# Performance work log

Hardware: AMD Instinct MI355X
Metric: run time of the kernel (lower is better)

Reference implementation:

```python
import jax, jax.numpy as jnp
import numpy as np
import math

D_MODEL = 512
NHEAD = 8
NUM_LAYERS = 3
FF_HIDDEN = 512
B, LQ, LK = 4, 1024, 2048
LN_EPS = 1e-5


def _mha(q_in, k_in, v_in, Wq, Wk, Wv, Wo, nhead, mask):
    # Weights stored [d_in, d_out]; torch Linear(bias=False) is x @ W.T, we fold the
    # transpose into storage so math is identical.
    Bq, Lq, d = q_in.shape
    dh = d // nhead
    # NOTE: original uses .view(B, nhead, -1, dh) on contiguous [B, L, d] — a plain
    # row-major reshape, NOT the usual transpose head split. Replicate exactly.
    q = (q_in @ Wq).reshape(Bq, nhead, -1, dh)
    k = (k_in @ Wk).reshape(Bq, nhead, -1, dh)
    v = (v_in @ Wv).reshape(Bq, nhead, -1, dh)
    u = jnp.einsum('bhqd,bhkd->bhqk', q, k) / math.sqrt(dh)
    if mask is not None:
        m = mask[:, None]  # broadcast over heads
        u = jnp.where(m, -jnp.inf, u)
    attn = jax.nn.softmax(u, axis=-1)
    if mask is not None:
        attn = jnp.where(m, 0.0, attn)
    out = jnp.einsum('bhqk,bhkd->bhqd', attn, v).reshape(Bq, Lq, d)
    return out @ Wo


def _layernorm(x, g, b):
    mu = jnp.mean(x, axis=-1, keepdims=True)
    var = jnp.mean((x - mu) ** 2, axis=-1, keepdims=True)
    return (x - mu) * jax.lax.rsqrt(var + LN_EPS) * g + b


def setup_inputs() -> dict:
    key = jax.random.key(0)
    ks = jax.random.split(key, 16)
    d, L, f = D_MODEL, NUM_LAYERS, FF_HIDDEN
    s = 0.02
    inp = {
        'x': jax.random.normal(ks[0], (B, LK, d), jnp.float32),
        'h': jax.random.normal(ks[1], (B, LQ, d), jnp.float32),
        'mask': jax.random.randint(ks[2], (B, LQ, LK), 0, 10) == 0,
        'wq': jax.random.normal(ks[3], (L, d, d), jnp.float32) * s,
        'wk': jax.random.normal(ks[4], (L, d, d), jnp.float32) * s,
        'wv': jax.random.normal(ks[5], (L, d, d), jnp.float32) * s,
        'wo': jax.random.normal(ks[6], (L, d, d), jnp.float32) * s,
        'ffw1': jax.random.normal(ks[7], (L, d, f), jnp.float32) * s,
        'ffb1': jnp.zeros((L, f), jnp.float32),
        'ffw2': jax.random.normal(ks[8], (L, f, d), jnp.float32) * s,
        'ffb2': jnp.zeros((L, d), jnp.float32),
        'g1': jnp.ones((L, d), jnp.float32),
        'be1': jnp.zeros((L, d), jnp.float32),
        'g2': jnp.ones((L, d), jnp.float32),
        'be2': jnp.zeros((L, d), jnp.float32),
        'out_wq': jax.random.normal(ks[9], (d, d), jnp.float32) * s,
        'out_wk': jax.random.normal(ks[10], (d, d), jnp.float32) * s,
    }
    return inp


def reference(x, h, mask, wq, wk, wv, wo, ffw1, ffb1, ffw2, ffb2, g1, be1, g2, be2, out_wq, out_wk):
    L = wq.shape[0]
    for i in range(L):
        a = _mha(h, x, x, wq[i], wk[i], wv[i], wo[i], NHEAD, mask)
        h = _layernorm(h + a, g1[i], be1[i])
        ff = jax.nn.relu(h @ ffw1[i] + ffb1[i]) @ ffw2[i] + ffb2[i]
        h = _layernorm(h + ff, g2[i], be2[i])
    # output MHA with nhead=1, output_attention=True: returns u.mean(dim=1)
    d = h.shape[-1]
    q = (h @ out_wq)[:, None]  # [B,1,Lq,d]
    k = (x @ out_wk)[:, None]  # [B,1,Lk,d]
    u = jnp.einsum('bhqd,bhkd->bhqk', q, k) / math.sqrt(d)
    # mean over head dim of size 1; torch .squeeze(1) is a no-op since Lq > 1
    return u.mean(axis=1)  # [B, Lq, Lk]
```

## Files before the change

kernel.cpp:

```cpp
#include <hip/hip_runtime.h>
#include <math.h>


#define D_MODEL 512
#define LQ 1024
#define LKK 2048
#define BB 4
#define NL 3
#define KSPLIT 2
#define NROWS 32768

typedef __bf16 bf16;
typedef __bf16 bf16x8 __attribute__((ext_vector_type(8)));
typedef __bf16 bf16x4 __attribute__((ext_vector_type(4)));
typedef float f32x4 __attribute__((ext_vector_type(4)));

__device__ inline f32x4 mfma16(bf16x8 a, bf16x8 b, f32x4 c) {
    return __builtin_amdgcn_mfma_f32_16x16x32_bf16(a, b, c, 0, 0, 0);
}

__device__ inline void gload16(const void* g, void* l) {
    __builtin_amdgcn_global_load_lds(
        (const __attribute__((address_space(1))) void*)g,
        (__attribute__((address_space(3))) void*)l, 16, 0, 0);
}

__global__ __launch_bounds__(256) void cast_kernel(
    const float* __restrict__ in, bf16* __restrict__ out, long n)
{
    long i4 = ((long)blockIdx.x * 256 + threadIdx.x) * 4;
    if (i4 >= n) return;
    float4 v = *(const float4*)(in + i4);
    bf16x4 o;
    o[0] = (bf16)v.x; o[1] = (bf16)v.y; o[2] = (bf16)v.z; o[3] = (bf16)v.w;
    *(bf16x4*)(out + i4) = o;
}

__global__ __launch_bounds__(256) void tcast_kernel(
    const float* __restrict__ in, bf16* __restrict__ out, long dstride)
{
    __shared__ float t[32][33];
    const float* ip = in + (long)blockIdx.z * 262144;
    bf16* op = out + (long)blockIdx.z * dstride;
    int tx = threadIdx.x & 31, ty = threadIdx.x >> 5;
    int x0 = blockIdx.x * 32, y0 = blockIdx.y * 32;
#pragma unroll
    for (int i = 0; i < 4; i++)
        t[ty + 8 * i][tx] = ip[(long)(y0 + ty + 8 * i) * 512 + x0 + tx];
    __syncthreads();
#pragma unroll
    for (int i = 0; i < 4; i++)
        op[(long)(x0 + ty + 8 * i) * 512 + y0 + tx] = (bf16)t[tx][ty + 8 * i];
}

__global__ __launch_bounds__(256) void maskbits_kernel(
    const int* __restrict__ m, unsigned* __restrict__ bits)
{
    long i = (long)blockIdx.x * 256 + threadIdx.x;
    int v = m[i] != 0;
    unsigned long long bal = __ballot(v);
    int lane = threadIdx.x & 63;
    if (lane == 0) bits[i >> 5] = (unsigned)bal;
    else if (lane == 32) bits[i >> 5] = (unsigned)(bal >> 32);
}

__global__ __launch_bounds__(256) void vtrans_kernel(
    const bf16* __restrict__ v, bf16* __restrict__ vt)
{
    __shared__ bf16 t[64][72];
    int bh = blockIdx.y;
    int p0 = blockIdx.x * 64;
    const bf16* vb = v + ((long)bh * 2048 + p0) * 64;
    bf16* vtb = vt + (long)bh * 64 * 2048;
    int tid = threadIdx.x;
#pragma unroll
    for (int it = 0; it < 2; it++) {
        int r = it * 32 + (tid >> 3);
        int c8 = (tid & 7) * 8;
        bf16x8 vv = *(const bf16x8*)(vb + (long)r * 64 + c8);
        *(bf16x8*)&t[r][c8] = vv;
    }
    __syncthreads();
#pragma unroll
    for (int it = 0; it < 2; it++) {
        int d = it * 32 + (tid >> 3);
        int p8 = (tid & 7) * 8;
        bf16x8 ov;
#pragma unroll
        for (int j = 0; j < 8; j++) ov[j] = t[p8 + j][d];
        *(bf16x8*)(vtb + (long)d * 2048 + p0 + p8) = ov;
    }
}

template<int BIAS, int RELU, int OUT_BF16>
__global__ __launch_bounds__(256) void mfma_gemm(
    const bf16* __restrict__ A, const bf16* __restrict__ Bt,
    const float* __restrict__ bias, void* __restrict__ Cv,
    int N, int K, float scale, long sA, long sB, long sC)
{
    __shared__ bf16 As[128][32];
    __shared__ bf16 Bs[64][32];
    int tid = threadIdx.x;
    int lane = tid & 63, w = tid >> 6;
    int wr = w >> 1, wc = w & 1;
    int g = lane >> 4, c = lane & 15;
    long z = blockIdx.z;
    const bf16* Ab = A + z * sA;
    const bf16* Bb = Bt + z * sB;
    long row0 = (long)blockIdx.y * 128;
    int n0 = blockIdx.x * 64;

    f32x4 acc[4][2];
#pragma unroll
    for (int m = 0; m < 4; m++)
#pragma unroll
        for (int n = 0; n < 2; n++) acc[m][n] = (f32x4){0.f, 0.f, 0.f, 0.f};

    for (int k0 = 0; k0 < K; k0 += 32) {
        __syncthreads();
        const bf16* ga = Ab + (row0 + w * 32 + (lane >> 2)) * K + k0 + (lane & 3) * 8;
        gload16(ga, &As[w * 32][0]);
        gload16(ga + (long)16 * K, &As[w * 32 + 16][0]);
        const bf16* gb = Bb + (long)(n0 + w * 16 + (lane >> 2)) * K + k0 + (lane & 3) * 8;
        gload16(gb, &Bs[w * 16][0]);
        __syncthreads();
        bf16x8 af[4], bfr[2];
#pragma unroll
        for (int m = 0; m < 4; m++)
            af[m] = *(const bf16x8*)&As[wr * 64 + m * 16 + c][g * 8];
#pragma unroll
        for (int n = 0; n < 2; n++)
            bfr[n] = *(const bf16x8*)&Bs[wc * 32 + n * 16 + c][g * 8];
#pragma unroll
        for (int m = 0; m < 4; m++)
#pragma unroll
            for (int n = 0; n < 2; n++)
                acc[m][n] = mfma16(af[m], bfr[n], acc[m][n]);
    }

    float bv[2] = {0.f, 0.f};
    if (BIAS) {
#pragma unroll
        for (int n = 0; n < 2; n++) bv[n] = bias[n0 + wc * 32 + n * 16 + c];
    }
    float* Cf = (float*)Cv + z * sC;
    bf16* Cb = (bf16*)Cv + z * sC;
#pragma unroll
    for (int m = 0; m < 4; m++)
#pragma unroll
        for (int n = 0; n < 2; n++)
#pragma unroll
            for (int j = 0; j < 4; j++) {
                long row = row0 + wr * 64 + m * 16 + g * 4 + j;
                int col = n0 + wc * 32 + n * 16 + c;
                float v = acc[m][n][j] * scale;
                if (BIAS) v += bv[n];
                if (RELU) v = fmaxf(v, 0.f);
                if (OUT_BF16) Cb[row * N + col] = (bf16)v;
                else Cf[row * N + col] = v;
            }
}

template<int OUT_BF16>
__global__ __launch_bounds__(256) void mfma_gemm128(
    const bf16* __restrict__ A, const bf16* __restrict__ Bt,
    void* __restrict__ Cv, int N, int K, float scale,
    long sA, long sB, long sC)
{
    __shared__ bf16 As[128][32];
    __shared__ bf16 Bs[128][32];
    int tid = threadIdx.x;
    int lane = tid & 63, w = tid >> 6;
    int wr = w >> 1, wc = w & 1;
    int g = lane >> 4, c = lane & 15;
    long z = blockIdx.z;
    const bf16* Ab = A + z * sA;
    const bf16* Bb = Bt + z * sB;
    long row0 = (long)blockIdx.y * 128;
    int n0 = blockIdx.x * 128;

    f32x4 acc[4][4];
#pragma unroll
    for (int m = 0; m < 4; m++)
#pragma unroll
        for (int n = 0; n < 4; n++) acc[m][n] = (f32x4){0.f, 0.f, 0.f, 0.f};

    for (int k0 = 0; k0 < K; k0 += 32) {
        __syncthreads();
        const bf16* ga = Ab + (row0 + w * 16 + (lane >> 2)) * K + k0 + (lane & 3) * 8;
        gload16(ga, &As[w * 16][0]);
        gload16(ga + (long)64 * K, &As[w * 16 + 64][0]);
        const bf16* gb = Bb + (long)(n0 + w * 16 + (lane >> 2)) * K + k0 + (lane & 3) * 8;
        gload16(gb, &Bs[w * 16][0]);
        gload16(gb + (long)64 * K, &Bs[w * 16 + 64][0]);
        __syncthreads();
        bf16x8 af[4], bfr[4];
#pragma unroll
        for (int m = 0; m < 4; m++)
            af[m] = *(const bf16x8*)&As[wr * 64 + m * 16 + c][g * 8];
#pragma unroll
        for (int n = 0; n < 4; n++)
            bfr[n] = *(const bf16x8*)&Bs[wc * 64 + n * 16 + c][g * 8];
#pragma unroll
        for (int m = 0; m < 4; m++)
#pragma unroll
            for (int n = 0; n < 4; n++)
                acc[m][n] = mfma16(af[m], bfr[n], acc[m][n]);
    }

    float* Cf = (float*)Cv + z * sC;
    bf16* Cb = (bf16*)Cv + z * sC;
#pragma unroll
    for (int m = 0; m < 4; m++)
#pragma unroll
        for (int n = 0; n < 4; n++)
#pragma unroll
            for (int j = 0; j < 4; j++) {
                long row = row0 + wr * 64 + m * 16 + g * 4 + j;
                int col = n0 + wc * 64 + n * 16 + c;
                float v = acc[m][n][j] * scale;
                if (OUT_BF16) Cb[row * N + col] = (bf16)v;
                else Cf[row * N + col] = v;
            }
}

__global__ __launch_bounds__(256, 4) void attn_mfma(
    const bf16* __restrict__ QP, const bf16* __restrict__ KP,
    const bf16* __restrict__ Vt, const unsigned* __restrict__ bits,
    bf16* __restrict__ Opart, float* __restrict__ Mpart,
    float* __restrict__ Lpart)
{
    __shared__ bf16 Kls[2][4096];
    __shared__ bf16 Vls[2][4096];
    __shared__ bf16 Pl[4][1024];

    int tid = threadIdx.x;
    int lane = tid & 63, wv = tid >> 6;
    int g = lane >> 4, c = lane & 15;

    int flat = blockIdx.x;
    int logical = (flat & 7) * 128 + (flat >> 3);
    int bh = logical >> 5;
    int rr = logical & 31;
    int sp = rr >> 4;
    int q0 = (rr & 15) * 64 + wv * 16;
    int b = bh >> 3;

    long qrow0 = (long)bh * 1024 + q0;
    long krow0 = (long)bh * 2048 + (long)sp * 1024;
    const bf16* vtb = Vt + (long)bh * 131072 + (long)sp * 1024;
    const unsigned* bitrow = bits + ((long)b * 1024 + q0 + c) * 64 + sp * 32;

    int lr = lane >> 3, lc = lane & 7;
    int scol = (lc ^ lr) * 8;
    int cs = c & 7;

    bf16x8 qa[2];
#pragma unroll
    for (int hh = 0; hh < 2; hh++)
        qa[hh] = *(const bf16x8*)(QP + (qrow0 + c) * 64 + hh * 32 + g * 8);

    f32x4 o_acc[4];
#pragma unroll
    for (int ot = 0; ot < 4; ot++) o_acc[ot] = (f32x4){0.f, 0.f, 0.f, 0.f};
    float m_r = -1e30f, l_r = 0.f;

    {
        const bf16* sk = KP + (krow0 + wv * 16 + lr) * 64 + scol;
        gload16(sk, &Kls[0][(wv * 16) * 64]);
        gload16(sk + 8 * 64, &Kls[0][(wv * 16 + 8) * 64]);
        const bf16* sv = vtb + (long)(wv * 16 + lr) * 2048 + scol;
        gload16(sv, &Vls[0][(wv * 16) * 64]);
        gload16(sv + 8 * 2048, &Vls[0][(wv * 16 + 8) * 64]);
    }
    uint2 wp_nxt = *(const uint2*)(bitrow);
    __syncthreads();

    const int NT = LKK / KSPLIT / 64;
    for (int kt = 0; kt < NT; kt++) {
        int cur = kt & 1;
        if (kt + 1 < NT) {
            int kn = (kt + 1) * 64;
            const bf16* sk = KP + (krow0 + kn + wv * 16 + lr) * 64 + scol;
            gload16(sk, &Kls[cur ^ 1][(wv * 16) * 64]);
            gload16(sk + 8 * 64, &Kls[cur ^ 1][(wv * 16 + 8) * 64]);
            const bf16* sv = vtb + (long)(wv * 16 + lr) * 2048 + kn + scol;
            gload16(sv, &Vls[cur ^ 1][(wv * 16) * 64]);
            gload16(sv + 8 * 2048, &Vls[cur ^ 1][(wv * 16 + 8) * 64]);
        }
        uint2 wp = wp_nxt;
        if (kt + 1 < NT) wp_nxt = *(const uint2*)(bitrow + (kt + 1) * 2);

        const char* kls = (const char*)&Kls[cur][0];
        f32x4 s[4];
#pragma unroll
        for (int mt = 0; mt < 4; mt++) {
            bf16x8 ka0 = *(const bf16x8*)(kls + (mt * 16 + c) * 128 + ((g ^ cs) << 4));
            bf16x8 ka1 = *(const bf16x8*)(kls + (mt * 16 + c) * 128 + (((4 + g) ^ cs) << 4));
            s[mt] = mfma16(ka0, qa[0], (f32x4){0.f, 0.f, 0.f, 0.f});
            s[mt] = mfma16(ka1, qa[1], s[mt]);
        }

#pragma unroll
        for (int mt = 0; mt < 4; mt++)
#pragma unroll
            for (int j = 0; j < 4; j++) {
                int kl = mt * 16 + 4 * g + j;
                unsigned wsel = (kl < 32) ? wp.x : wp.y;
                s[mt][j] = ((wsel >> (kl & 31)) & 1) ? -1e30f : s[mt][j] * 0.125f;
            }

        float mx = -1e30f;
#pragma unroll
        for (int mt = 0; mt < 4; mt++)
            mx = fmaxf(mx, fmaxf(fmaxf(s[mt][0], s[mt][1]),
                                 fmaxf(s[mt][2], s[mt][3])));
        mx = fmaxf(mx, __shfl_xor(mx, 16, 64));
        mx = fmaxf(mx, __shfl_xor(mx, 32, 64));

        float fct = 1.f;
        if (__any(mx > m_r + 8.f)) {
            float mnew = fmaxf(m_r, mx);
            fct = __expf(m_r - mnew);
            m_r = mnew;
            float fq[4];
#pragma unroll
            for (int j = 0; j < 4; j++)
                fq[j] = __shfl(fct, (lane & 48) | (4 * g + j), 64);
#pragma unroll
            for (int ot = 0; ot < 4; ot++)
#pragma unroll
                for (int j = 0; j < 4; j++) o_acc[ot][j] *= fq[j];
        }

        float sum = 0.f;
#pragma unroll
        for (int mt = 0; mt < 4; mt++)
#pragma unroll
            for (int j = 0; j < 4; j++) {
                float p = __expf(s[mt][j] - m_r);
                s[mt][j] = p;
                sum += p;
            }
        sum += __shfl_xor(sum, 16, 64);
        sum += __shfl_xor(sum, 32, 64);
        l_r = l_r * fct + sum;

        char* plb = (char*)&Pl[wv][0];
#pragma unroll
        for (int mt = 0; mt < 4; mt++) {
            bf16x4 pk;
#pragma unroll
            for (int j = 0; j < 4; j++) pk[j] = (bf16)s[mt][j];
            int wch = (mt * 2 + (g >> 1)) ^ cs;
            *(bf16x4*)(plb + c * 128 + (wch << 4) + (g & 1) * 8) = pk;
        }

        const char* vls = (const char*)&Vls[cur][0];
#pragma unroll
        for (int kh = 0; kh < 2; kh++) {
            bf16x8 pa = *(const bf16x8*)(plb + c * 128 + ((((kh << 2) + g) ^ cs) << 4));
#pragma unroll
            for (int ot = 0; ot < 4; ot++) {
                bf16x8 vbf = *(const bf16x8*)
                    (vls + (ot * 16 + c) * 128 + ((((kh << 2) + g) ^ cs) << 4));
                o_acc[ot] = mfma16(pa, vbf, o_acc[ot]);
            }
        }
        __syncthreads();
    }

    long ob = ((long)sp * NROWS + qrow0) * 64;
#pragma unroll
    for (int ot = 0; ot < 4; ot++)
#pragma unroll
        for (int j = 0; j < 4; j++)
            Opart[ob + (long)(4 * g + j) * 64 + ot * 16 + c] = (bf16)o_acc[ot][j];
    if (g == 0) {
        Mpart[(long)sp * NROWS + qrow0 + c] = m_r;
        Lpart[(long)sp * NROWS + qrow0 + c] = l_r;
    }
}

__global__ __launch_bounds__(256) void attn_combine(
    const bf16* __restrict__ Op, const float* __restrict__ Mp,
    const float* __restrict__ Lp, bf16* __restrict__ O)
{
    long idx = (long)blockIdx.x * 256 + threadIdx.x;
    long row = idx >> 6;
    float m0 = Mp[row], m1 = Mp[NROWS + row];
    float l0 = Lp[row], l1 = Lp[NROWS + row];
    float mm = fmaxf(m0, m1);
    float e0 = __expf(m0 - mm), e1 = __expf(m1 - mm);
    float inv = 1.f / (l0 * e0 + l1 * e1);
    float o = ((float)Op[idx] * e0 + (float)Op[(long)NROWS * 64 + idx] * e1) * inv;
    O[idx] = (bf16)o;
}

__global__ __launch_bounds__(256) void ln_kernel(
    const float* __restrict__ res, const float* __restrict__ y,
    const float* __restrict__ g, const float* __restrict__ bb,
    float* __restrict__ outf, bf16* __restrict__ outb)
{
    int wave = threadIdx.x >> 6, lane = threadIdx.x & 63;
    long row = (long)blockIdx.x * 4 + wave;
    const float* rp = res + row * D_MODEL;
    const float* yp = y + row * D_MODEL;
    float v[8];
    float s = 0.f, sq = 0.f;
#pragma unroll
    for (int j = 0; j < 8; j++) {
        int col = lane + 64 * j;
        v[j] = rp[col] + yp[col];
        s += v[j]; sq += v[j] * v[j];
    }
#pragma unroll
    for (int o = 32; o > 0; o >>= 1) {
        s += __shfl_down(s, o, 64);
        sq += __shfl_down(sq, o, 64);
    }
    s = __shfl(s, 0, 64);
    sq = __shfl(sq, 0, 64);
    float mean = s * (1.f / 512.f);
    float var = sq * (1.f / 512.f) - mean * mean;
    float rstd = rsqrtf(fmaxf(var, 0.f) + 1e-5f);
    float* opf = outf + row * D_MODEL;
    bf16* opb = outb + row * D_MODEL;
#pragma unroll
    for (int j = 0; j < 8; j++) {
        int col = lane + 64 * j;
        float o = (v[j] - mean) * rstd * g[col] + bb[col];
        opf[col] = o;
        opb[col] = (bf16)o;
    }
}

extern "C" void kernel_launch(void* const* d_in, const int* in_sizes, int n_in,
                              void* d_out, int out_size, void* d_ws, size_t ws_size,
                              hipStream_t stream)
{
    const float* x    = (const float*)d_in[0];
    const float* hin  = (const float*)d_in[1];
    const int*   mask = (const int*)d_in[2];
    const float* wq   = (const float*)d_in[3];
    const float* wk   = (const float*)d_in[4];
    const float* wv   = (const float*)d_in[5];
    const float* wo   = (const float*)d_in[6];
    const float* ffw1 = (const float*)d_in[7];
    const float* ffb1 = (const float*)d_in[8];
    const float* ffw2 = (const float*)d_in[9];
    const float* ffb2 = (const float*)d_in[10];
    const float* g1   = (const float*)d_in[11];
    const float* be1  = (const float*)d_in[12];
    const float* g2   = (const float*)d_in[13];
    const float* be2  = (const float*)d_in[14];
    const float* out_wq = (const float*)d_in[15];
    const float* out_wk = (const float*)d_in[16];
    float* out = (float*)d_out;

    const long NQ = (long)BB * LQ;
    const long NK = (long)BB * LKK;
    const long WSZ = 512L * 512;

    char* W = (char*)d_ws;
    float* h_f  = (float*)(W);
    char*  SH   = W + 8388608;
    float* y_f  = (float*)SH;
    bf16*  v_pl = (bf16*)SH;
    bf16*  opart= (bf16*)SH;
    bf16*  h_b  = (bf16*)(W + 16777216);
    bf16*  x_b  = (bf16*)(W + 20971520);
    bf16*  q_b  = (bf16*)(W + 29360128);
    bf16*  a_b  = (bf16*)(W + 33554432);
    bf16*  k_pl = (bf16*)(W + 37748736);
    bf16*  vt   = (bf16*)(W + 46137344);
    bf16*  wts  = (bf16*)(W + 54525952);
    bf16*  wtQ  = wts;
    bf16*  wtO  = wts + 3 * WSZ;
    bf16*  wtF1 = wts + 6 * WSZ;
    bf16*  wtF2 = wts + 9 * WSZ;
    bf16*  wtKV = wts + 12 * WSZ;
    bf16*  wtOQ = wts + 19 * WSZ;
    unsigned* mb = (unsigned*)(W + 65011712);
    float* Mpart = (float*)(W + 66060288);
    float* Lpart = (float*)(W + 66322432);

    const long sKV = ((bf16*)SH) - k_pl;

    dim3 blk(256);

    hipMemcpyAsync(h_f, hin, NQ * D_MODEL * sizeof(float),
                   hipMemcpyDeviceToDevice, stream);
    cast_kernel<<<dim3((NK * D_MODEL / 4 + 255) / 256), blk, 0, stream>>>(x, x_b, NK * D_MODEL);
    cast_kernel<<<dim3((NQ * D_MODEL / 4 + 255) / 256), blk, 0, stream>>>(hin, h_b, NQ * D_MODEL);
    dim3 gt(16, 16, 3);
    tcast_kernel<<<gt, blk, 0, stream>>>(wq, wtQ, WSZ);
    tcast_kernel<<<gt, blk, 0, stream>>>(wo, wtO, WSZ);
    tcast_kernel<<<gt, blk, 0, stream>>>(ffw1, wtF1, WSZ);
    tcast_kernel<<<gt, blk, 0, stream>>>(ffw2, wtF2, WSZ);
    tcast_kernel<<<gt, blk, 0, stream>>>(wk, wtKV, 2 * WSZ);
    tcast_kernel<<<gt, blk, 0, stream>>>(wv, wtKV + WSZ, 2 * WSZ);
    dim3 gt1(16, 16, 1);
    tcast_kernel<<<gt1, blk, 0, stream>>>(out_wk, wtKV + 6 * WSZ, 0);
    tcast_kernel<<<gt1, blk, 0, stream>>>(out_wq, wtOQ, 0);
    maskbits_kernel<<<dim3(32768), blk, 0, stream>>>(mask, mb);

    dim3 gq(8, 32, 1);
    dim3 gkv(4, 64, 2);
    dim3 gvt(32, 32);
    dim3 ga(1024);
    dim3 gc(NROWS * 64 / 256);

    for (int i = 0; i < NL; i++) {
        mfma_gemm<0,0,1><<<gq, blk, 0, stream>>>(h_b, wtQ + i * WSZ, nullptr, q_b,
            512, 512, 1.f, 0, 0, 0);
        mfma_gemm128<1><<<gkv, blk, 0, stream>>>(x_b, wtKV + 2 * i * WSZ, k_pl,
            512, 512, 1.f, 0, WSZ, sKV);
        vtrans_kernel<<<gvt, blk, 0, stream>>>(v_pl, vt);

        attn_mfma<<<ga, blk, 0, stream>>>(q_b, k_pl, vt, mb, opart, Mpart, Lpart);
        attn_combine<<<gc, blk, 0, stream>>>(opart, Mpart, Lpart, a_b);

        mfma_gemm<0,0,0><<<gq, blk, 0, stream>>>(a_b, wtO + i * WSZ, nullptr, y_f,
            512, 512, 1.f, 0, 0, 0);
        ln_kernel<<<dim3(NQ / 4), blk, 0, stream>>>(h_f, y_f,
            g1 + i * D_MODEL, be1 + i * D_MODEL, h_f, h_b);

        mfma_gemm<1,1,1><<<gq, blk, 0, stream>>>(h_b, wtF1 + i * WSZ,
            ffb1 + i * D_MODEL, q_b, 512, 512, 1.f, 0, 0, 0);
        mfma_gemm<1,0,0><<<gq, blk, 0, stream>>>(q_b, wtF2 + i * WSZ,
            ffb2 + i * D_MODEL, y_f, 512, 512, 1.f, 0, 0, 0);
        ln_kernel<<<dim3(NQ / 4), blk, 0, stream>>>(h_f, y_f,
            g2 + i * D_MODEL, be2 + i * D_MODEL, h_f, h_b);
    }

    mfma_gemm<0,0,1><<<gq, blk, 0, stream>>>(h_b, wtOQ, nullptr, q_b,
        512, 512, 1.f, 0, 0, 0);
    dim3 gkf(4, 64, 1);
    mfma_gemm128<1><<<gkf, blk, 0, stream>>>(x_b, wtKV + 6 * WSZ, k_pl,
        512, 512, 1.f, 0, 0, 0);
    dim3 gf(LKK / 128, LQ / 128, BB);
    mfma_gemm128<0><<<gf, blk, 0, stream>>>(q_b, k_pl, out,
        LKK, 512, 0.04419417382415922f,
        (long)LQ * 512, (long)LKK * 512, (long)LQ * LKK);
}
```

Before: 475.3 us.

## Double-buffer GEMM LDS tiles, fuse QKV projections, merge weight casts, use exp2

Both GEMM kernels now double-buffer their LDS tiles, so the next K-slice is prefetched while MFMAs run on the current one, leaving one barrier per iteration. The Q, K and V projections per layer, and the final Q/K projections, go through a single fused 128-tile kernel launch instead of separate launches. The eight weight transpose-cast launches become one kernel, and attention softmax switches to exp2 with the log2e factor folded into the scale and rescale threshold. The costs are twice the LDS per block, which may lower occupancy, and branchy per-z dispatch inside the fused kernels.

```diff
diff --git a/kernel.cpp b/kernel.cpp
--- a/kernel.cpp
+++ b/kernel.cpp
@@ -9,6 +9,7 @@
 #define NL 3
 #define KSPLIT 2
 #define NROWS 32768
+#define WSZC 262144L
 
 typedef __bf16 bf16;
 typedef __bf16 bf16x8 __attribute__((ext_vector_type(8)));
@@ -36,21 +37,34 @@
     *(bf16x4*)(out + i4) = o;
 }
 
-__global__ __launch_bounds__(256) void tcast_kernel(
-    const float* __restrict__ in, bf16* __restrict__ out, long dstride)
+__global__ __launch_bounds__(256) void tcast_all(
+    const float* __restrict__ wq, const float* __restrict__ wo,
+    const float* __restrict__ f1, const float* __restrict__ f2,
+    const float* __restrict__ wk, const float* __restrict__ wv,
+    const float* __restrict__ owq, const float* __restrict__ owk,
+    bf16* __restrict__ wts, bf16* __restrict__ wtOQ)
 {
     __shared__ float t[32][33];
-    const float* ip = in + (long)blockIdx.z * 262144;
-    bf16* op = out + (long)blockIdx.z * dstride;
+    int z = blockIdx.z;
+    const float* src; bf16* dst;
+    if (z < 3)       { src = wq  + z * WSZC;        dst = wts + (long)z * WSZC; }
+    else if (z < 6)  { src = wo  + (z - 3) * WSZC;  dst = wts + (long)z * WSZC; }
+    else if (z < 9)  { src = f1  + (z - 6) * WSZC;  dst = wts + (long)z * WSZC; }
+    else if (z < 12) { src = f2  + (z - 9) * WSZC;  dst = wts + (long)z * WSZC; }
+    else if (z < 15) { src = wk  + (z - 12) * WSZC; dst = wts + (12 + 2 * (z - 12)) * WSZC; }
+    else if (z < 18) { src = wv  + (z - 15) * WSZC; dst = wts + (13 + 2 * (z - 15)) * WSZC; }
+    else if (z == 18){ src = owq;                   dst = wtOQ; }
+    else             { src = owk;                   dst = wts + 18 * WSZC; }
+
     int tx = threadIdx.x & 31, ty = threadIdx.x >> 5;
     int x0 = blockIdx.x * 32, y0 = blockIdx.y * 32;
 #pragma unroll
     for (int i = 0; i < 4; i++)
-        t[ty + 8 * i][tx] = ip[(long)(y0 + ty + 8 * i) * 512 + x0 + tx];
+        t[ty + 8 * i][tx] = src[(long)(y0 + ty + 8 * i) * 512 + x0 + tx];
     __syncthreads();
 #pragma unroll
     for (int i = 0; i < 4; i++)
-        op[(long)(x0 + ty + 8 * i) * 512 + y0 + tx] = (bf16)t[tx][ty + 8 * i];
+        dst[(long)(x0 + ty + 8 * i) * 512 + y0 + tx] = (bf16)t[tx][ty + 8 * i];
 }
 
 __global__ __launch_bounds__(256) void maskbits_kernel(
@@ -96,17 +110,14 @@
 __global__ __launch_bounds__(256) void mfma_gemm(
     const bf16* __restrict__ A, const bf16* __restrict__ Bt,
     const float* __restrict__ bias, void* __restrict__ Cv,
-    int N, int K, float scale, long sA, long sB, long sC)
-{
-    __shared__ bf16 As[128][32];
-    __shared__ bf16 Bs[64][32];
+    int N, int K)
+{
+    __shared__ bf16 As[2][4096];
+    __shared__ bf16 Bs[2][2048];
     int tid = threadIdx.x;
     int lane = tid & 63, w = tid >> 6;
     int wr = w >> 1, wc = w & 1;
     int g = lane >> 4, c = lane & 15;
-    long z = blockIdx.z;
-    const bf16* Ab = A + z * sA;
-    const bf16* Bb = Bt + z * sB;
     long row0 = (long)blockIdx.y * 128;
     int n0 = blockIdx.x * 64;
 
@@ -116,26 +127,34 @@
 #pragma unroll
         for (int n = 0; n < 2; n++) acc[m][n] = (f32x4){0.f, 0.f, 0.f, 0.f};
 
-    for (int k0 = 0; k0 < K; k0 += 32) {
-        __syncthreads();
-        const bf16* ga = Ab + (row0 + w * 32 + (lane >> 2)) * K + k0 + (lane & 3) * 8;
-        gload16(ga, &As[w * 32][0]);
-        gload16(ga + (long)16 * K, &As[w * 32 + 16][0]);
-        const bf16* gb = Bb + (long)(n0 + w * 16 + (lane >> 2)) * K + k0 + (lane & 3) * 8;
-        gload16(gb, &Bs[w * 16][0]);
-        __syncthreads();
+    int lr4 = lane >> 2, lc8 = (lane & 3) * 8;
+    auto STAGE = [&](int buf, int k0) {
+        const bf16* ga = A + (row0 + w * 32 + lr4) * (long)K + k0 + lc8;
+        gload16(ga, &As[buf][(w * 32) * 32]);
+        gload16(ga + (long)16 * K, &As[buf][(w * 32 + 16) * 32]);
+        const bf16* gb = Bt + (long)(n0 + w * 16 + lr4) * K + k0 + lc8;
+        gload16(gb, &Bs[buf][(w * 16) * 32]);
+    };
+
+    STAGE(0, 0);
+    __syncthreads();
+    int nk = K >> 5;
+    for (int it = 0; it < nk; ++it) {
+        int cur = it & 1;
+        if (it + 1 < nk) STAGE(cur ^ 1, (it + 1) << 5);
         bf16x8 af[4], bfr[2];
 #pragma unroll
         for (int m = 0; m < 4; m++)
-            af[m] = *(const bf16x8*)&As[wr * 64 + m * 16 + c][g * 8];
+            af[m] = *(const bf16x8*)&As[cur][(wr * 64 + m * 16 + c) * 32 + g * 8];
 #pragma unroll
         for (int n = 0; n < 2; n++)
-            bfr[n] = *(const bf16x8*)&Bs[wc * 32 + n * 16 + c][g * 8];
+            bfr[n] = *(const bf16x8*)&Bs[cur][(wc * 32 + n * 16 + c) * 32 + g * 8];
 #pragma unroll
         for (int m = 0; m < 4; m++)
 #pragma unroll
             for (int n = 0; n < 2; n++)
                 acc[m][n] = mfma16(af[m], bfr[n], acc[m][n]);
+        __syncthreads();
     }
 
     float bv[2] = {0.f, 0.f};
@@ -143,8 +162,8 @@
 #pragma unroll
         for (int n = 0; n < 2; n++) bv[n] = bias[n0 + wc * 32 + n * 16 + c];
     }
-    float* Cf = (float*)Cv + z * sC;
-    bf16* Cb = (bf16*)Cv + z * sC;
+    float* Cf = (float*)Cv;
+    bf16* Cb = (bf16*)Cv;
 #pragma unroll
     for (int m = 0; m < 4; m++)
 #pragma unroll
@@ -153,7 +172,7 @@
             for (int j = 0; j < 4; j++) {
                 long row = row0 + wr * 64 + m * 16 + g * 4 + j;
                 int col = n0 + wc * 32 + n * 16 + c;
-                float v = acc[m][n][j] * scale;
+                float v = acc[m][n][j];
                 if (BIAS) v += bv[n];
                 if (RELU) v = fmaxf(v, 0.f);
                 if (OUT_BF16) Cb[row * N + col] = (bf16)v;
@@ -162,22 +181,17 @@
 }
 
 template<int OUT_BF16>
-__global__ __launch_bounds__(256) void mfma_gemm128(
-    const bf16* __restrict__ A, const bf16* __restrict__ Bt,
+__device__ inline void gemm128_body(
+    const bf16* __restrict__ Ab, const bf16* __restrict__ Bb,
     void* __restrict__ Cv, int N, int K, float scale,
-    long sA, long sB, long sC)
-{
-    __shared__ bf16 As[128][32];
-    __shared__ bf16 Bs[128][32];
+    long row0, int n0)
+{
+    __shared__ bf16 As[2][4096];
+    __shared__ bf16 Bs[2][4096];
     int tid = threadIdx.x;
     int lane = tid & 63, w = tid >> 6;
     int wr = w >> 1, wc = w & 1;
     int g = lane >> 4, c = lane & 15;
-    long z = blockIdx.z;
-    const bf16* Ab = A + z * sA;
-    const bf16* Bb = Bt + z * sB;
-    long row0 = (long)blockIdx.y * 128;
-    int n0 = blockIdx.x * 128;
 
     f32x4 acc[4][4];
 #pragma unroll
@@ -185,31 +199,39 @@
 #pragma unroll
         for (int n = 0; n < 4; n++) acc[m][n] = (f32x4){0.f, 0.f, 0.f, 0.f};
 
-    for (int k0 = 0; k0 < K; k0 += 32) {
-        __syncthreads();
-        const bf16* ga = Ab + (row0 + w * 16 + (lane >> 2)) * K + k0 + (lane & 3) * 8;
-        gload16(ga, &As[w * 16][0]);
-        gload16(ga + (long)64 * K, &As[w * 16 + 64][0]);
-        const bf16* gb = Bb + (long)(n0 + w * 16 + (lane >> 2)) * K + k0 + (lane & 3) * 8;
-        gload16(gb, &Bs[w * 16][0]);
-        gload16(gb + (long)64 * K, &Bs[w * 16 + 64][0]);
-        __syncthreads();
+    int lr4 = lane >> 2, lc8 = (lane & 3) * 8;
+    auto STAGE = [&](int buf, int k0) {
+        const bf16* ga = Ab + (row0 + w * 16 + lr4) * (long)K + k0 + lc8;
+        gload16(ga, &As[buf][(w * 16) * 32]);
+        gload16(ga + (long)64 * K, &As[buf][(w * 16 + 64) * 32]);
+        const bf16* gb = Bb + (long)(n0 + w * 16 + lr4) * K + k0 + lc8;
+        gload16(gb, &Bs[buf][(w * 16) * 32]);
+        gload16(gb + (long)64 * K, &Bs[buf][(w * 16 + 64) * 32]);
+    };
+
+    STAGE(0, 0);
+    __syncthreads();
+    int nk = K >> 5;
+    for (int it = 0; it < nk; ++it) {
+        int cur = it & 1;
+        if (it + 1 < nk) STAGE(cur ^ 1, (it + 1) << 5);
         bf16x8 af[4], bfr[4];
 #pragma unroll
         for (int m = 0; m < 4; m++)
-            af[m] = *(const bf16x8*)&As[wr * 64 + m * 16 + c][g * 8];
+            af[m] = *(const bf16x8*)&As[cur][(wr * 64 + m * 16 + c) * 32 + g * 8];
 #pragma unroll
         for (int n = 0; n < 4; n++)
-            bfr[n] = *(const bf16x8*)&Bs[wc * 64 + n * 16 + c][g * 8];
+            bfr[n] = *(const bf16x8*)&Bs[cur][(wc * 64 + n * 16 + c) * 32 + g * 8];
 #pragma unroll
         for (int m = 0; m < 4; m++)
 #pragma unroll
             for (int n = 0; n < 4; n++)
                 acc[m][n] = mfma16(af[m], bfr[n], acc[m][n]);
-    }
-
-    float* Cf = (float*)Cv + z * sC;
-    bf16* Cb = (bf16*)Cv + z * sC;
+        __syncthreads();
+    }
+
+    float* Cf = (float*)Cv;
+    bf16* Cb = (bf16*)Cv;
 #pragma unroll
     for (int m = 0; m < 4; m++)
 #pragma unroll
@@ -224,6 +246,31 @@
             }
 }
 
+__global__ __launch_bounds__(256) void mfma_gemm128(
+    const bf16* __restrict__ A, const bf16* __restrict__ Bt,
+    float* __restrict__ Cv, int N, int K, float scale,
+    long sA, long sB, long sC)
+{
+    long z = blockIdx.z;
+    gemm128_body<0>(A + z * sA, Bt + z * sB, Cv + z * sC, N, K, scale,
+                    (long)blockIdx.y * 128, blockIdx.x * 128);
+}
+
+__global__ __launch_bounds__(256) void qkv_gemm(
+    const bf16* __restrict__ Ah, const bf16* __restrict__ Ax,
+    const bf16* __restrict__ B0, const bf16* __restrict__ B1,
+    const bf16* __restrict__ B2,
+    bf16* __restrict__ C0, bf16* __restrict__ C1, bf16* __restrict__ C2)
+{
+    int z = blockIdx.z;
+    if (z == 0 && blockIdx.y >= 32) return;
+    const bf16* A = z ? Ax : Ah;
+    const bf16* Bt = (z == 0) ? B0 : (z == 1 ? B1 : B2);
+    bf16* C = (z == 0) ? C0 : (z == 1 ? C1 : C2);
+    gemm128_body<1>(A, Bt, C, 512, 512, 1.f,
+                    (long)blockIdx.y * 128, blockIdx.x * 128);
+}
+
 __global__ __launch_bounds__(256, 4) void attn_mfma(
     const bf16* __restrict__ QP, const bf16* __restrict__ KP,
     const bf16* __restrict__ Vt, const unsigned* __restrict__ bits,
@@ -233,6 +280,8 @@
     __shared__ bf16 Kls[2][4096];
     __shared__ bf16 Vls[2][4096];
     __shared__ bf16 Pl[4][1024];
+
+    const float C2 = 0.1803368801111243f;
 
     int tid = threadIdx.x;
     int lane = tid & 63, wv = tid >> 6;
@@ -307,7 +356,7 @@
             for (int j = 0; j < 4; j++) {
                 int kl = mt * 16 + 4 * g + j;
                 unsigned wsel = (kl < 32) ? wp.x : wp.y;
-                s[mt][j] = ((wsel >> (kl & 31)) & 1) ? -1e30f : s[mt][j] * 0.125f;
+                s[mt][j] = ((wsel >> (kl & 31)) & 1) ? -1e30f : s[mt][j] * C2;
             }
 
         float mx = -1e30f;
@@ -319,9 +368,9 @@
         mx = fmaxf(mx, __shfl_xor(mx, 32, 64));
 
         float fct = 1.f;
-        if (__any(mx > m_r + 8.f)) {
+        if (__any(mx > m_r + 11.5415f)) {
             float mnew = fmaxf(m_r, mx);
-            fct = __expf(m_r - mnew);
+            fct = exp2f(m_r - mnew);
             m_r = mnew;
             float fq[4];
 #pragma unroll
@@ -338,7 +387,7 @@
         for (int mt = 0; mt < 4; mt++)
 #pragma unroll
             for (int j = 0; j < 4; j++) {
-                float p = __expf(s[mt][j] - m_r);
+                float p = exp2f(s[mt][j] - m_r);
                 s[mt][j] = p;
                 sum += p;
             }
@@ -391,7 +440,7 @@
     float m0 = Mp[row], m1 = Mp[NROWS + row];
     float l0 = Lp[row], l1 = Lp[NROWS + row];
     float mm = fmaxf(m0, m1);
-    float e0 = __expf(m0 - mm), e1 = __expf(m1 - mm);
+    float e0 = exp2f(m0 - mm), e1 = exp2f(m1 - mm);
     float inv = 1.f / (l0 * e0 + l1 * e1);
     float o = ((float)Op[idx] * e0 + (float)Op[(long)NROWS * 64 + idx] * e1) * inv;
     O[idx] = (bf16)o;
@@ -460,7 +509,6 @@
 
     const long NQ = (long)BB * LQ;
     const long NK = (long)BB * LKK;
-    const long WSZ = 512L * 512;
 
     char* W = (char*)d_ws;
     float* h_f  = (float*)(W);
@@ -475,17 +523,10 @@
     bf16*  k_pl = (bf16*)(W + 37748736);
     bf16*  vt   = (bf16*)(W + 46137344);
     bf16*  wts  = (bf16*)(W + 54525952);
-    bf16*  wtQ  = wts;
-    bf16*  wtO  = wts + 3 * WSZ;
-    bf16*  wtF1 = wts + 6 * WSZ;
-    bf16*  wtF2 = wts + 9 * WSZ;
-    bf16*  wtKV = wts + 12 * WSZ;
-    bf16*  wtOQ = wts + 19 * WSZ;
+    bf16*  wtOQ = wts + 19 * WSZC;
     unsigned* mb = (unsigned*)(W + 65011712);
     float* Mpart = (float*)(W + 66060288);
     float* Lpart = (float*)(W + 66322432);
-
-    const long sKV = ((bf16*)SH) - k_pl;
 
     dim3 blk(256);
 
@@ -493,54 +534,44 @@
                    hipMemcpyDeviceToDevice, stream);
     cast_kernel<<<dim3((NK * D_MODEL / 4 + 255) / 256), blk, 0, stream>>>(x, x_b, NK * D_MODEL);
     cast_kernel<<<dim3((NQ * D_MODEL / 4 + 255) / 256), blk, 0, stream>>>(hin, h_b, NQ * D_MODEL);
-    dim3 gt(16, 16, 3);
-    tcast_kernel<<<gt, blk, 0, stream>>>(wq, wtQ, WSZ);
-    tcast_kernel<<<gt, blk, 0, stream>>>(wo, wtO, WSZ);
-    tcast_kernel<<<gt, blk, 0, stream>>>(ffw1, wtF1, WSZ);
-    tcast_kernel<<<gt, blk, 0, stream>>>(ffw2, wtF2, WSZ);
-    tcast_kernel<<<gt, blk, 0, stream>>>(wk, wtKV, 2 * WSZ);
-    tcast_kernel<<<gt, blk, 0, stream>>>(wv, wtKV + WSZ, 2 * WSZ);
-    dim3 gt1(16, 16, 1);
-    tcast_kernel<<<gt1, blk, 0, stream>>>(out_wk, wtKV + 6 * WSZ, 0);
-    tcast_kernel<<<gt1, blk, 0, stream>>>(out_wq, wtOQ, 0);
+    tcast_all<<<dim3(16, 16, 20), blk, 0, stream>>>(
+        wq, wo, ffw1, ffw2, wk, wv, out_wq, out_wk, wts, wtOQ);
     maskbits_kernel<<<dim3(32768), blk, 0, stream>>>(mask, mb);
 
     dim3 gq(8, 32, 1);
-    dim3 gkv(4, 64, 2);
+    dim3 gqkv(4, 64, 3);
     dim3 gvt(32, 32);
     dim3 ga(1024);
     dim3 gc(NROWS * 64 / 256);
 
     for (int i = 0; i < NL; i++) {
-        mfma_gemm<0,0,1><<<gq, blk, 0, stream>>>(h_b, wtQ + i * WSZ, nullptr, q_b,
-            512, 512, 1.f, 0, 0, 0);
-        mfma_gemm128<1><<<gkv, blk, 0, stream>>>(x_b, wtKV + 2 * i * WSZ, k_pl,
-            512, 512, 1.f, 0, WSZ, sKV);
+        qkv_gemm<<<gqkv, blk, 0, stream>>>(h_b, x_b,
+            wts + i * WSZC, wts + (12 + 2 * i) * WSZC, wts + (13 + 2 * i) * WSZC,
+            q_b, k_pl, v_pl);
         vtrans_kernel<<<gvt, blk, 0, stream>>>(v_pl, vt);
 
         attn_mfma<<<ga, blk, 0, stream>>>(q_b, k_pl, vt, mb, opart, Mpart, Lpart);
         attn_combine<<<gc, blk, 0, stream>>>(opart, Mpart, Lpart, a_b);
 
-        mfma_gemm<0,0,0><<<gq, blk, 0, stream>>>(a_b, wtO + i * WSZ, nullptr, y_f,
-            512, 512, 1.f, 0, 0, 0);
+        mfma_gemm<0,0,0><<<gq, blk, 0, stream>>>(a_b, wts + (3 + i) * WSZC,
+            nullptr, y_f, 512, 512);
         ln_kernel<<<dim3(NQ / 4), blk, 0, stream>>>(h_f, y_f,
             g1 + i * D_MODEL, be1 + i * D_MODEL, h_f, h_b);
 
-        mfma_gemm<1,1,1><<<gq, blk, 0, stream>>>(h_b, wtF1 + i * WSZ,
-            ffb1 + i * D_MODEL, q_b, 512, 512, 1.f, 0, 0, 0);
-        mfma_gemm<1,0,0><<<gq, blk, 0, stream>>>(q_b, wtF2 + i * WSZ,
-            ffb2 + i * D_MODEL, y_f, 512, 512, 1.f, 0, 0, 0);
+        mfma_gemm<1,1,1><<<gq, blk, 0, stream>>>(h_b, wts + (6 + i) * WSZC,
+            ffb1 + i * D_MODEL, q_b, 512, 512);
+        mfma_gemm<1,0,0><<<gq, blk, 0, stream>>>(q_b, wts + (9 + i) * WSZC,
+            ffb2 + i * D_MODEL, y_f, 512, 512);
         ln_kernel<<<dim3(NQ / 4), blk, 0, stream>>>(h_f, y_f,
             g2 + i * D_MODEL, be2 + i * D_MODEL, h_f, h_b);
     }
 
-    mfma_gemm<0,0,1><<<gq, blk, 0, stream>>>(h_b, wtOQ, nullptr, q_b,
-        512, 512, 1.f, 0, 0, 0);
-    dim3 gkf(4, 64, 1);
-    mfma_gemm128<1><<<gkf, blk, 0, stream>>>(x_b, wtKV + 6 * WSZ, k_pl,
-        512, 512, 1.f, 0, 0, 0);
+    dim3 gqk(4, 64, 2);
+    qkv_gemm<<<gqk, blk, 0, stream>>>(h_b, x_b,
+        wtOQ, wts + 18 * WSZC, wts + 18 * WSZC, q_b, k_pl, k_pl);
+
     dim3 gf(LKK / 128, LQ / 128, BB);
-    mfma_gemm128<0><<<gf, blk, 0, stream>>>(q_b, k_pl, out,
+    mfma_gemm128<<<gf, blk, 0, stream>>>(q_b, k_pl, out,
         LKK, 512, 0.04419417382415922f,
         (long)LQ * 512, (long)LKK * 512, (long)LQ * LKK);
 }
```

New measurement: 430.2 us. -9.5%, faster.
